# Performance work log

Measured on AMD Instinct MI355X. Metric: run time of the kernel, lower is better.

Reference implementation:

```python
import jax, jax.numpy as jnp
import numpy as np

BETA = 0.25  # commitment-loss weight (kwargs['beta'])


def setup_inputs() -> dict:
    key = jax.random.key(0)
    k1, k2 = jax.random.split(key)
    B, C, H, W = 16, 256, 64, 64
    K = 2048
    feats = jax.random.normal(k1, (B, C, H, W), dtype=jnp.float32)
    # nn.Embedding init: uniform(-1/n_codewords, 1/codeword_dim)
    codebook = jax.random.uniform(k2, (K, C), minval=-1.0 / K, maxval=1.0 / C,
                                  dtype=jnp.float32)
    return {"feats": feats, "codebook": codebook}


def reference(feats, codebook):
    B, C, H, W = feats.shape
    K = codebook.shape[0]
    z = jnp.transpose(feats, (0, 2, 3, 1))          # [B,H,W,C]
    zf = z.reshape(-1, C)                            # [N,C], N=B*H*W
    # squared-euclidean distances via ||z||^2 + ||e||^2 - 2 z.e : [N,K]
    d = (jnp.sum(zf * zf, axis=1, keepdims=True)
         + jnp.sum(codebook * codebook, axis=1)
         - 2.0 * (zf @ codebook.T))
    min_encoding_indices = jnp.argmin(d, axis=1)     # [N]
    mat_id_probs = jax.nn.softmax(-jnp.abs(d), axis=1)  # [N,K]
    z_q = codebook[min_encoding_indices].reshape(z.shape)  # [B,H,W,C]
    loss = (BETA * jnp.mean((jax.lax.stop_gradient(z_q) - z) ** 2)
            + jnp.mean((z_q - jax.lax.stop_gradient(z)) ** 2))
    # straight-through estimator
    z_q_st = z + jax.lax.stop_gradient(z_q - z)
    z_q_out = jnp.transpose(z_q_st, (0, 3, 1, 2))    # [B,C,H,W]
    idx_out = min_encoding_indices.reshape(B, H, W)
    probs_out = jnp.transpose(mat_id_probs.reshape(B, H, W, K), (0, 3, 1, 2))
    return z_q_out, idx_out, loss, probs_out
```

## Files before the change

kernel.cpp:

```cpp
#include <hip/hip_runtime.h>

#define HW 4096
#define CC 256
#define KK 2048
#define BB 16
#define NN (BB*HW)
#define RPB 128

#define ZQ_SZ   (BB*CC*HW)
#define IDX_OFF ZQ_SZ
#define LOSS_OFF (IDX_OFF + NN)
#define PROBS_OFF (LOSS_OFF + 1)

#define EH_OFF 0
#define EE_OFF 262144
#define EXT_OFF 264192
#define ZZ_OFF 280576
#define MS_OFF 346112
#define SS_OFF 477184
#define IKEY_OFF 608256

#define TAU 0.01f
#define CAND_CAP 512
#define KTC 32
#define KT_N 32
#define CS_N 17

typedef short bf16x8 __attribute__((ext_vector_type(8)));
typedef float f32x16 __attribute__((ext_vector_type(16)));
typedef unsigned int u32;
typedef unsigned long long u64;

__device__ __forceinline__ void gload16(const void* g, void* l){
  __builtin_amdgcn_global_load_lds(
      (const __attribute__((address_space(1))) u32*)g,
      (__attribute__((address_space(3))) u32*)l, 16, 0, 0);
}

__device__ __forceinline__ unsigned short bf16rn(float x){
  unsigned u = __float_as_uint(x);
  return (unsigned short)((u + 0x7fffu + ((u >> 16) & 1u)) >> 16);
}

template<int STRIDE>
__device__ __forceinline__ float np_sumsq256(const float* __restrict__ a){
  float res0 = 0.f, res1 = 0.f;
  #pragma unroll
  for (int h = 0; h < 2; h++){
    const float* p = a + (size_t)h * 128 * STRIDE;
    float r[8];
    #pragma unroll
    for (int j = 0; j < 8; j++){ float x = p[(size_t)j * STRIDE]; r[j] = __fmul_rn(x, x); }
    for (int i = 8; i < 128; i += 8){
      #pragma unroll
      for (int j = 0; j < 8; j++){
        float x = p[(size_t)(i + j) * STRIDE];
        r[j] = __fadd_rn(r[j], __fmul_rn(x, x));
      }
    }
    float s = __fadd_rn(__fadd_rn(__fadd_rn(r[0], r[1]), __fadd_rn(r[2], r[3])),
                        __fadd_rn(__fadd_rn(r[4], r[5]), __fadd_rn(r[6], r[7])));
    if (h == 0) res0 = s; else res1 = s;
  }
  return __fadd_rn(res0, res1);
}

__global__ void k_prep2(const float* __restrict__ cb, float* __restrict__ out){
  const int k = blockIdx.x * 256 + threadIdx.x;
  unsigned short* eh = (unsigned short*)(out + EH_OFF);
  unsigned short* ex = (unsigned short*)(out + EXT_OFF);
  const float* row = cb + (size_t)k * CC;
  for (int c = 0; c < CC; c++) eh[k * CC + c] = bf16rn(row[c]);
  float ee = np_sumsq256<1>(row);
  out[EE_OFF + k] = ee;
  ex[k * 16] = bf16rn(-0.5f * ee);
  #pragma unroll
  for (int j = 1; j < 16; ++j) ex[k * 16 + j] = 0;
}

__global__ void k_zz(const float* __restrict__ feats, float* __restrict__ out){
  const int n = blockIdx.x * 256 + threadIdx.x;
  const int b = n >> 12, hw = n & 4095;
  out[ZZ_OFF + n] = np_sumsq256<HW>(feats + (size_t)b * CC * HW + hw);
}


#define GEMM_PROLOG \
  const int t = threadIdx.x; \
  const int w = t >> 6, l = t & 63; \
  const int grp = l >> 5; \
  const int lane31 = l & 31; \
  const int bid = blockIdx.x; \
  const int rb = bid >> 1, h = bid & 1; \
  const int n0 = rb * RPB; \
  const int bi = n0 >> 12; \
  const int hw0 = n0 & 4095; \
  const int myhw = hw0 + w * 32 + lane31; \
  bf16x8 ah0[16], ahx; \
  { \
    const float* zb = feats + (size_t)bi * CC * HW + myhw; \
    _Pragma("unroll") \
    for (int cs = 0; cs < 16; ++cs){ \
      _Pragma("unroll") \
      for (int j = 0; j < 8; ++j) \
        ah0[cs][j] = (short)bf16rn(zb[(size_t)(cs * 16 + grp * 8 + j) * HW]); \
    } \
    _Pragma("unroll") \
    for (int j = 0; j < 8; ++j) ahx[j] = 0; \
    if (grp == 0) ahx[0] = (short)0x3F80; \
  } \
  const unsigned short* ehg = (const unsigned short*)(out + EH_OFF) + (size_t)h * 1024 * CC; \
  const unsigned short* exg = (const unsigned short*)(out + EXT_OFF) + (size_t)h * 1024 * 16; \
  int ofs_[4]; \
  _Pragma("unroll") \
  for (int i = 0; i < 4; ++i){ \
    int ix = i * 256 + t; \
    int cd = ix & 31, g = (ix >> 5) & 1, cs = ix >> 6; \
    ofs_[i] = cd * CC + cs * 16 + g * 8; \
  } \
  int x_ofs = 0; \
  if (t < 64){ int cd = t & 31, g = (t >> 5) & 1; x_ofs = cd * 16 + g * 8; }

#define STAGE(KT, B) { \
    const size_t kto_ = (size_t)(KT) * (KTC * CC); \
    _Pragma("unroll") \
    for (int i_ = 0; i_ < 4; ++i_) \
      gload16(ehg + ofs_[i_] + kto_, &lds_e[B][(i_ * 256 + t) * 16]); \
    if (t < 64) \
      gload16(exg + x_ofs + (size_t)(KT) * (KTC * 16), &lds_e[B][(1024 + t) * 16]); }

#define COMPUTE(B) { \
    _Pragma("unroll") \
    for (int ii = 0; ii < 16; ++ii){ accA[ii] = 0.f; accB[ii] = 0.f; } \
    _Pragma("unroll") \
    for (int cs = 0; cs < 16; ++cs){ \
      const unsigned char* bp_ = &lds_e[B][(size_t)(cs * 2 + grp) * 512 + lane31 * 16]; \
      bf16x8 e_ = *(const bf16x8*)(bp_); \
      if (cs & 1) accB = __builtin_amdgcn_mfma_f32_32x32x16_bf16(e_, ah0[cs], accB, 0, 0, 0); \
      else        accA = __builtin_amdgcn_mfma_f32_32x32x16_bf16(e_, ah0[cs], accA, 0, 0, 0); \
    } \
    { \
      const unsigned char* bp_ = &lds_e[B][(size_t)(32 + grp) * 512 + lane31 * 16]; \
      bf16x8 e_ = *(const bf16x8*)(bp_); \
      accA = __builtin_amdgcn_mfma_f32_32x32x16_bf16(e_, ahx, accA, 0, 0, 0); \
    } }

__global__ __launch_bounds__(256, 4)
void k_stats(const float* __restrict__ feats, float* __restrict__ out){
  __shared__ __align__(16) unsigned char lds_e[2][CS_N * 2 * KTC * 16];
  GEMM_PROLOG
  f32x16 accA, accB;
  float m0 = 3e38f, ss0 = 0.f;

  STAGE(0, 0);
  __syncthreads();
  for (int kt = 0; kt < KT_N; ++kt){
    const int buf = kt & 1;
    if (kt < KT_N - 1) STAGE(kt + 1, buf ^ 1);
    COMPUTE(buf);
    #pragma unroll
    for (int r = 0; r < 16; ++r){
      float s = -2.f * (accA[r] + accB[r]);
      m0 = fminf(m0, s);
      ss0 += __expf(-s);
    }
    __syncthreads();
  }
  m0 = fminf(m0, __shfl_xor(m0, 32));
  ss0 += __shfl_xor(ss0, 32);
  if (grp == 0){
    out[MS_OFF + h * NN + n0 + w * 32 + lane31] = m0;
    out[SS_OFF + h * NN + n0 + w * 32 + lane31] = ss0;
  }
}

__global__ __launch_bounds__(256, 4)
void k_probs(const float* __restrict__ feats, const float* __restrict__ cb,
             float* __restrict__ out){
  __shared__ __align__(16) unsigned char lds_e[2][CS_N * 2 * KTC * 16];
  __shared__ int cand[CAND_CAP];
  __shared__ int cand_n;
  GEMM_PROLOG
  if (t == 0) cand_n = 0;
  f32x16 accA, accB;

  const int myrow = n0 + w * 32 + lane31;
  float m0, inv0;
  {
    float ma = out[MS_OFF + myrow], mb = out[MS_OFF + NN + myrow];
    float sa = out[SS_OFF + myrow], sb = out[SS_OFF + NN + myrow];
    m0 = fminf(ma, mb);
    inv0 = 1.f / (sa + sb);
  }

  STAGE(0, 0);
  __syncthreads();
  for (int kt = 0; kt < KT_N; ++kt){
    const int buf = kt & 1;
    if (kt < KT_N - 1) STAGE(kt + 1, buf ^ 1);
    COMPUTE(buf);
    float* pb = out + (size_t)PROBS_OFF
              + (size_t)(bi * KK + h * 1024 + kt * KTC + 4 * grp) * HW + myhw;
    #pragma unroll
    for (int r = 0; r < 16; ++r){
      int off = (r & 3) + 8 * (r >> 2);
      float s = -2.f * (accA[r] + accB[r]);
      pb[(size_t)off * HW] = __expf(-s) * inv0;
      if (s <= m0 + TAU){
        int sl = atomicAdd(&cand_n, 1);
        if (sl < CAND_CAP)
          cand[sl] = ((w * 32 + lane31) << 16) | (h * 1024 + kt * KTC + 4 * grp + off);
      }
    }
    __syncthreads();
  }

  u64* ikey = (u64*)(out + IKEY_OFF);
  int nc = cand_n; if (nc > CAND_CAP) nc = CAND_CAP;
  for (int i = t; i < nc; i += 256){
    int rc = cand[i];
    int rl = (rc >> 16) & 127, code = rc & 2047;
    int n = n0 + rl;
    const float* zp = feats + (size_t)(n >> 12) * CC * HW + (n & 4095);
    const float* ep = cb + (size_t)code * CC;
    float a = 0.f;
    #pragma unroll 8
    for (int c = 0; c < CC; ++c) a = __builtin_fmaf(zp[(size_t)c * HW], ep[c], a);
    float t1 = __fadd_rn(out[ZZ_OFF + n], out[EE_OFF + code]);
    float d = __fadd_rn(t1, -2.f * a);
    u64 key = ((u64)__float_as_uint(d) << 32) | (unsigned)code;
    atomicMin(&ikey[n], key);
  }
}

__global__ void k_final(const float* __restrict__ feats, const float* __restrict__ cb,
                        float* __restrict__ out){
  const int t = threadIdx.x;
  const int n = blockIdx.x * 256 + t;
  const u64* ikey = (const u64*)(out + IKEY_OFF);
  int code = (int)(ikey[n] & 2047u);
  out[IDX_OFF + n] = (float)code;
  const int bi = n >> 12, hw = n & 4095;
  const float* ep = cb + (size_t)code * CC;
  const float* zp = feats + (size_t)bi * CC * HW + hw;
  float s = 0.f;
  for (int c = 0; c < CC; ++c){
    float dz = ep[c] - zp[(size_t)c * HW];
    s = __builtin_fmaf(dz, dz, s);
  }
  #pragma unroll
  for (int off = 32; off; off >>= 1) s += __shfl_xor(s, off);
  if ((t & 63) == 0) atomicAdd(out + LOSS_OFF, s * (1.25f / 16777216.f));
}

__global__ void k_zq(const float* __restrict__ cb, float* __restrict__ out){
  const int f4 = blockIdx.x * 256 + threadIdx.x;
  const int f = f4 * 4;
  const int b = f >> 20;
  const int rem = f & 1048575;
  const int c = rem >> 12;
  const int hw = rem & 4095;
  const int n = b * HW + hw;
  const float* idxf = out + IDX_OFF;
  float4 iv = *(const float4*)(idxf + n);
  float4 o;
  o.x = cb[(size_t)((int)iv.x) * CC + c];
  o.y = cb[(size_t)((int)iv.y) * CC + c];
  o.z = cb[(size_t)((int)iv.z) * CC + c];
  o.w = cb[(size_t)((int)iv.w) * CC + c];
  *(float4*)(out + f) = o;
}

extern "C" void kernel_launch(void* const* d_in, const int* in_sizes, int n_in,
                              void* d_out, int out_size, void* d_ws, size_t ws_size,
                              hipStream_t stream){
  const float* feats = (const float*)d_in[0];
  const float* cb    = (const float*)d_in[1];
  float* out = (float*)d_out;

  (void)hipMemsetAsync(out + LOSS_OFF, 0, sizeof(float), stream);
  (void)hipMemsetAsync(out + IKEY_OFF, 0xFF, (size_t)NN * 8, stream);
  hipLaunchKernelGGL(k_prep2, dim3(8),     dim3(256), 0, stream, cb, out);
  hipLaunchKernelGGL(k_zz,    dim3(256),   dim3(256), 0, stream, feats, out);
  hipLaunchKernelGGL(k_stats, dim3(1024),  dim3(256), 0, stream, feats, out);
  hipLaunchKernelGGL(k_probs, dim3(1024),  dim3(256), 0, stream, feats, cb, out);
  hipLaunchKernelGGL(k_final, dim3(256),   dim3(256), 0, stream, feats, cb, out);
  hipLaunchKernelGGL(k_zq,    dim3(16384), dim3(256), 0, stream, cb, out);
}
```

Measured before the change: 534.4 us.

## Triple-buffer codebook tiles with partial vmcnt barriers and parallelize bf16 conversion

Both GEMM kernels now keep three LDS stages in flight instead of two. The full __syncthreads is replaced by an s_waitcnt vmcnt(N) plus s_barrier, so newer prefetches and probs stores can stay outstanding while the current tile is consumed. Launch bounds drop to 3 and 2 waves-per-EU to fit the larger LDS footprint. The serial per-thread codebook bf16 conversion is split into a wide vectorized k_cvt kernel and a small k_ee kernel. Risks: the hand-counted vmcnt values must match the actual number of outstanding memory ops, and occupancy is lower.

```diff
diff --git a/kernel.cpp b/kernel.cpp
--- a/kernel.cpp
+++ b/kernel.cpp
@@ -25,6 +25,7 @@
 #define KTC 32
 #define KT_N 32
 #define CS_N 17
+#define HB 17408
 
 typedef short bf16x8 __attribute__((ext_vector_type(8)));
 typedef float f32x16 __attribute__((ext_vector_type(16)));
@@ -41,6 +42,10 @@
   unsigned u = __float_as_uint(x);
   return (unsigned short)((u + 0x7fffu + ((u >> 16) & 1u)) >> 16);
 }
+
+#define PB(n0, n1) { \
+  if (t < 64) asm volatile("s_waitcnt vmcnt(" n0 ")\n\ts_barrier" ::: "memory"); \
+  else        asm volatile("s_waitcnt vmcnt(" n1 ")\n\ts_barrier" ::: "memory"); }
 
 template<int STRIDE>
 __device__ __forceinline__ float np_sumsq256(const float* __restrict__ a){
@@ -65,13 +70,20 @@
   return __fadd_rn(res0, res1);
 }
 
-__global__ void k_prep2(const float* __restrict__ cb, float* __restrict__ out){
+__global__ void k_cvt(const float* __restrict__ cb, float* __restrict__ out){
+  const int i = blockIdx.x * 256 + threadIdx.x;
+  const int k = i >> 5, c8 = (i & 31) * 8;
+  const float* row = cb + (size_t)k * CC + c8;
+  unsigned short v[8];
+  #pragma unroll
+  for (int j = 0; j < 8; ++j) v[j] = bf16rn(row[j]);
+  *(uint4*)((unsigned short*)(out + EH_OFF) + (size_t)k * CC + c8) = *(uint4*)v;
+}
+
+__global__ void k_ee(const float* __restrict__ cb, float* __restrict__ out){
   const int k = blockIdx.x * 256 + threadIdx.x;
-  unsigned short* eh = (unsigned short*)(out + EH_OFF);
   unsigned short* ex = (unsigned short*)(out + EXT_OFF);
-  const float* row = cb + (size_t)k * CC;
-  for (int c = 0; c < CC; c++) eh[k * CC + c] = bf16rn(row[c]);
-  float ee = np_sumsq256<1>(row);
+  float ee = np_sumsq256<1>(cb + (size_t)k * CC);
   out[EE_OFF + k] = ee;
   ex[k * 16] = bf16rn(-0.5f * ee);
   #pragma unroll
@@ -121,50 +133,57 @@
   int x_ofs = 0; \
   if (t < 64){ int cd = t & 31, g = (t >> 5) & 1; x_ofs = cd * 16 + g * 8; }
 
-#define STAGE(KT, B) { \
+#define STAGE(KT, BI) { \
+    unsigned char* bb_ = lds_e + (size_t)(BI) * HB; \
     const size_t kto_ = (size_t)(KT) * (KTC * CC); \
     _Pragma("unroll") \
     for (int i_ = 0; i_ < 4; ++i_) \
-      gload16(ehg + ofs_[i_] + kto_, &lds_e[B][(i_ * 256 + t) * 16]); \
+      gload16(ehg + ofs_[i_] + kto_, bb_ + (i_ * 256 + t) * 16); \
     if (t < 64) \
-      gload16(exg + x_ofs + (size_t)(KT) * (KTC * 16), &lds_e[B][(1024 + t) * 16]); }
-
-#define COMPUTE(B) { \
+      gload16(exg + x_ofs + (size_t)(KT) * (KTC * 16), bb_ + (1024 + t) * 16); }
+
+#define COMPUTE(BI) { \
+    const unsigned char* hb_ = lds_e + (size_t)(BI) * HB; \
     _Pragma("unroll") \
     for (int ii = 0; ii < 16; ++ii){ accA[ii] = 0.f; accB[ii] = 0.f; } \
     _Pragma("unroll") \
     for (int cs = 0; cs < 16; ++cs){ \
-      const unsigned char* bp_ = &lds_e[B][(size_t)(cs * 2 + grp) * 512 + lane31 * 16]; \
+      const unsigned char* bp_ = hb_ + (size_t)(cs * 2 + grp) * 512 + lane31 * 16; \
       bf16x8 e_ = *(const bf16x8*)(bp_); \
       if (cs & 1) accB = __builtin_amdgcn_mfma_f32_32x32x16_bf16(e_, ah0[cs], accB, 0, 0, 0); \
       else        accA = __builtin_amdgcn_mfma_f32_32x32x16_bf16(e_, ah0[cs], accA, 0, 0, 0); \
     } \
     { \
-      const unsigned char* bp_ = &lds_e[B][(size_t)(32 + grp) * 512 + lane31 * 16]; \
+      const unsigned char* bp_ = hb_ + (size_t)(32 + grp) * 512 + lane31 * 16; \
       bf16x8 e_ = *(const bf16x8*)(bp_); \
       accA = __builtin_amdgcn_mfma_f32_32x32x16_bf16(e_, ahx, accA, 0, 0, 0); \
     } }
 
-__global__ __launch_bounds__(256, 4)
+__global__ __launch_bounds__(256, 3)
 void k_stats(const float* __restrict__ feats, float* __restrict__ out){
-  __shared__ __align__(16) unsigned char lds_e[2][CS_N * 2 * KTC * 16];
+  __shared__ __align__(16) unsigned char lds_e[3 * HB];
   GEMM_PROLOG
   f32x16 accA, accB;
   float m0 = 3e38f, ss0 = 0.f;
 
   STAGE(0, 0);
-  __syncthreads();
+  STAGE(1, 1);
+  PB("5", "4")
+
+  int cur = 0, nxt = 2;
   for (int kt = 0; kt < KT_N; ++kt){
-    const int buf = kt & 1;
-    if (kt < KT_N - 1) STAGE(kt + 1, buf ^ 1);
-    COMPUTE(buf);
+    if (kt + 2 < KT_N) STAGE(kt + 2, nxt);
+    COMPUTE(cur);
     #pragma unroll
     for (int r = 0; r < 16; ++r){
       float s = -2.f * (accA[r] + accB[r]);
       m0 = fminf(m0, s);
       ss0 += __expf(-s);
     }
-    __syncthreads();
+    cur = cur == 2 ? 0 : cur + 1;
+    nxt = nxt == 2 ? 0 : nxt + 1;
+    if (kt == KT_N - 1) break;
+    if (kt < KT_N - 2){ PB("5", "4") } else { PB("0", "0") }
   }
   m0 = fminf(m0, __shfl_xor(m0, 32));
   ss0 += __shfl_xor(ss0, 32);
@@ -174,10 +193,10 @@
   }
 }
 
-__global__ __launch_bounds__(256, 4)
+__global__ __launch_bounds__(256, 2)
 void k_probs(const float* __restrict__ feats, const float* __restrict__ cb,
              float* __restrict__ out){
-  __shared__ __align__(16) unsigned char lds_e[2][CS_N * 2 * KTC * 16];
+  __shared__ __align__(16) unsigned char lds_e[3 * HB];
   __shared__ int cand[CAND_CAP];
   __shared__ int cand_n;
   GEMM_PROLOG
@@ -194,11 +213,13 @@
   }
 
   STAGE(0, 0);
-  __syncthreads();
+  STAGE(1, 1);
+  PB("5", "4")
+
+  int cur = 0, nxt = 2;
   for (int kt = 0; kt < KT_N; ++kt){
-    const int buf = kt & 1;
-    if (kt < KT_N - 1) STAGE(kt + 1, buf ^ 1);
-    COMPUTE(buf);
+    if (kt + 2 < KT_N) STAGE(kt + 2, nxt);
+    COMPUTE(cur);
     float* pb = out + (size_t)PROBS_OFF
               + (size_t)(bi * KK + h * 1024 + kt * KTC + 4 * grp) * HW + myhw;
     #pragma unroll
@@ -212,8 +233,14 @@
           cand[sl] = ((w * 32 + lane31) << 16) | (h * 1024 + kt * KTC + 4 * grp + off);
       }
     }
-    __syncthreads();
-  }
+    cur = cur == 2 ? 0 : cur + 1;
+    nxt = nxt == 2 ? 0 : nxt + 1;
+    if (kt == KT_N - 1) break;
+    if (kt == 0)            { PB("21", "20") }
+    else if (kt < KT_N - 2) { PB("37", "36") }
+    else                    { PB("16", "16") }
+  }
+  __syncthreads();
 
   u64* ikey = (u64*)(out + IKEY_OFF);
   int nc = cand_n; if (nc > CAND_CAP) nc = CAND_CAP;
@@ -280,7 +307,8 @@
 
   (void)hipMemsetAsync(out + LOSS_OFF, 0, sizeof(float), stream);
   (void)hipMemsetAsync(out + IKEY_OFF, 0xFF, (size_t)NN * 8, stream);
-  hipLaunchKernelGGL(k_prep2, dim3(8),     dim3(256), 0, stream, cb, out);
+  hipLaunchKernelGGL(k_cvt,   dim3(256),   dim3(256), 0, stream, cb, out);
+  hipLaunchKernelGGL(k_ee,    dim3(8),     dim3(256), 0, stream, cb, out);
   hipLaunchKernelGGL(k_zz,    dim3(256),   dim3(256), 0, stream, feats, out);
   hipLaunchKernelGGL(k_stats, dim3(1024),  dim3(256), 0, stream, feats, out);
   hipLaunchKernelGGL(k_probs, dim3(1024),  dim3(256), 0, stream, feats, cb, out);
```

Result: faster. 517.5 us (-3.2%).
